# Optimization experiments

Measured on AMD Instinct MI355X. Metric: run time of the kernel, lower is better.

Reference implementation:

```python
import jax, jax.numpy as jnp
import numpy as np

B, I, S = 1024, 128, 512
UNFOLDS = 6


def setup_inputs() -> dict:
    key = jax.random.key(0)
    ks = jax.random.split(key, 16)
    inputs = jax.random.normal(ks[0], (B, I), dtype=jnp.float32)
    hx = jax.random.normal(ks[1], (B, S), dtype=jnp.float32)
    # learned parameters, initialized per _get_variables()
    input_w = jnp.ones((I,), dtype=jnp.float32)
    input_b = jnp.zeros((I,), dtype=jnp.float32)
    sensory_mu = jax.random.uniform(ks[2], (I, S)) * 0.5 + 0.3
    sensory_sigma = jax.random.uniform(ks[3], (I, S)) * 5.0 + 3.0
    sensory_W = jax.random.uniform(ks[4], (I, S), minval=0.01, maxval=1.0)
    sensory_erev = (2.0 * jax.random.randint(ks[5], (I, S), 0, 2) - 1.0).astype(jnp.float32)
    mu = jax.random.uniform(ks[6], (S, S)) * 0.5 + 0.3
    sigma = jax.random.uniform(ks[7], (S, S)) * 5.0 + 3.0
    W = jax.random.uniform(ks[8], (S, S), minval=0.01, maxval=1.0)
    erev = (2.0 * jax.random.randint(ks[9], (S, S), 0, 2) - 1.0).astype(jnp.float32)
    vleak = jax.random.uniform(ks[10], (S,)) * 0.4 - 0.2
    gleak = jnp.ones((S,), dtype=jnp.float32)   # gleak_init_min == gleak_init_max == 1
    cm_t = jnp.full((S,), 0.5, dtype=jnp.float32)  # cm_init_min == cm_init_max == 0.5
    return dict(inputs=inputs, hx=hx, input_w=input_w, input_b=input_b,
                sensory_mu=sensory_mu, sensory_sigma=sensory_sigma,
                sensory_W=sensory_W, sensory_erev=sensory_erev,
                mu=mu, sigma=sigma, W=W, erev=erev,
                vleak=vleak, gleak=gleak, cm_t=cm_t)


def reference(inputs, hx, input_w, input_b, sensory_mu, sensory_sigma,
              sensory_W, sensory_erev, mu, sigma, W, erev, vleak, gleak, cm_t):
    # Affine input mapping
    x = inputs * input_w + input_b                      # [B, I]
    # Sensory synapse activation (computed once): [B, I, S]
    sens_act = sensory_W * jax.nn.sigmoid(sensory_sigma * (x[:, :, None] - sensory_mu))
    w_num_sensory = jnp.sum(sens_act * sensory_erev, axis=1)  # [B, S]
    w_den_sensory = jnp.sum(sens_act, axis=1)                 # [B, S]

    v = hx
    for _ in range(UNFOLDS):
        # Recurrent synapse activation: broadcast state over presynaptic dim -> [B, S, S]
        w_act = W * jax.nn.sigmoid(sigma * (v[:, :, None] - mu))
        w_num = jnp.sum(w_act * erev, axis=1) + w_num_sensory   # [B, S]
        w_den = jnp.sum(w_act, axis=1) + w_den_sensory          # [B, S]
        numerator = cm_t * v + gleak * vleak + w_num
        denominator = cm_t + gleak + w_den
        v = numerator / denominator
    # forward returns (outputs, next_state), which are the same tensor
    return v
```

## Files before the change

### kernel.cpp

```cpp
#include <hip/hip_runtime.h>
#include <hip/hip_bf16.h>
#include <math.h>


#define B_TOT 1024
#define I_DIM 128
#define S_DIM 512
#define UNFOLDS 6
#define BT 4
#define TBL_N 4096
#define T_MAX 14.0f

__global__ __launch_bounds__(256) void prep_kernel(
    const float* __restrict__ sens_mu, const float* __restrict__ sens_sigma,
    const float* __restrict__ sens_W, const float* __restrict__ sens_erev,
    const float* __restrict__ mu, const float* __restrict__ sigma,
    const float* __restrict__ W, const float* __restrict__ erev,
    float4* __restrict__ recP, float4* __restrict__ sensP)
{
    const float L2E   = 1.4426950408889634f;
    const float SCALE = (float)TBL_N / (2.0f * T_MAX);
    const float OFF   = (float)(TBL_N / 2) + 0.5f;
    int idx = blockIdx.x * 256 + threadIdx.x;
    if (idx < I_DIM * S_DIM) {
        float sg = sens_sigma[idx], m = sens_mu[idx], w = sens_W[idx], er = sens_erev[idx];
        float A = -sg * L2E, C = sg * m * L2E;
        sensP[idx] = make_float4(A * SCALE, C * SCALE + OFF, w * er, w);
    }
    if (idx < S_DIM * S_DIM) {
        float sg = sigma[idx], m = mu[idx], w = W[idx], er = erev[idx];
        float A = -sg * L2E, C = sg * m * L2E;
        recP[idx] = make_float4(A * SCALE, C * SCALE + OFF, w * er, w);
    }
}

__global__ __launch_bounds__(512, 2) void liquid_main(
    const float* __restrict__ inputs,
    const float* __restrict__ hx,
    const float* __restrict__ input_w,
    const float* __restrict__ input_b,
    const float4* __restrict__ sensP,
    const float4* __restrict__ recP,
    const float* __restrict__ vleak,
    const float* __restrict__ gleak,
    const float* __restrict__ cm_t,
    float* __restrict__ out)
{
    const int j = threadIdx.x;
    const int b0 = blockIdx.x * BT;

    __shared__ float tbl[TBL_N];
    __shared__ float xs[BT][I_DIM];
    __shared__ float vs[BT][S_DIM];

    {
        const float INV_SCALE = (2.0f * T_MAX) / (float)TBL_N;
        for (int k = threadIdx.x; k < TBL_N; k += S_DIM) {
            float tc = ((float)k - (float)(TBL_N / 2)) * INV_SCALE;
            tbl[k] = 1.0f / (1.0f + exp2f(tc));
        }
    }

    {
        int b = threadIdx.x >> 7, ii = threadIdx.x & 127;
        xs[b][ii] = inputs[(b0 + b) * I_DIM + ii] * input_w[ii] + input_b[ii];
    }
    #pragma unroll
    for (int k = 0; k < BT; ++k)
        vs[k][j] = hx[(b0 + k) * S_DIM + j];
    __syncthreads();

    const float CLHI = (float)(TBL_N - 1);

    float snum[BT], sden[BT];
    #pragma unroll
    for (int b = 0; b < BT; ++b) { snum[b] = 0.f; sden[b] = 0.f; }

    for (int i = 0; i < I_DIM; i += 4) {
        float4 p[4];
        #pragma unroll
        for (int u = 0; u < 4; ++u) p[u] = sensP[(i + u) * S_DIM + j];
        #pragma unroll
        for (int b = 0; b < BT; ++b) {
            float4 xv4 = *(const float4*)&xs[b][i];
            float xv[4] = {xv4.x, xv4.y, xv4.z, xv4.w};
            #pragma unroll
            for (int u = 0; u < 4; ++u) {
                float f = fmaf(p[u].x, xv[u], p[u].y);
                f = __builtin_amdgcn_fmed3f(f, 0.0f, CLHI);
                float s = tbl[(unsigned)f];
                snum[b] = fmaf(p[u].z, s, snum[b]);
                sden[b] = fmaf(p[u].w, s, sden[b]);
            }
        }
    }

    const float gl = gleak[j], vl = vleak[j], cmj = cm_t[j];
    const float glvl = gl * vl;
    const float cg = cmj + gl;

    for (int it = 0; it < UNFOLDS; ++it) {
        float num[BT], den[BT];
        #pragma unroll
        for (int b = 0; b < BT; ++b) { num[b] = snum[b]; den[b] = sden[b]; }

        for (int i = 0; i < S_DIM; i += 4) {
            float4 p[4];
            #pragma unroll
            for (int u = 0; u < 4; ++u) p[u] = recP[(i + u) * S_DIM + j];
            #pragma unroll
            for (int b = 0; b < BT; ++b) {
                float4 vv4 = *(const float4*)&vs[b][i];
                float vv[4] = {vv4.x, vv4.y, vv4.z, vv4.w};
                #pragma unroll
                for (int u = 0; u < 4; ++u) {
                    float f = fmaf(p[u].x, vv[u], p[u].y);
                    f = __builtin_amdgcn_fmed3f(f, 0.0f, CLHI);
                    float s = tbl[(unsigned)f];
                    num[b] = fmaf(p[u].z, s, num[b]);
                    den[b] = fmaf(p[u].w, s, den[b]);
                }
            }
        }

        float vnew[BT];
        #pragma unroll
        for (int b = 0; b < BT; ++b) {
            float vold = vs[b][j];
            vnew[b] = (fmaf(cmj, vold, glvl) + num[b]) / (cg + den[b]);
        }
        __syncthreads();
        #pragma unroll
        for (int b = 0; b < BT; ++b) vs[b][j] = vnew[b];
        __syncthreads();
    }

    #pragma unroll
    for (int b = 0; b < BT; ++b)
        out[(b0 + b) * S_DIM + j] = vs[b][j];
}

extern "C" void kernel_launch(void* const* d_in, const int* in_sizes, int n_in,
                              void* d_out, int out_size, void* d_ws, size_t ws_size,
                              hipStream_t stream) {
    const float* inputs   = (const float*)d_in[0];
    const float* hx       = (const float*)d_in[1];
    const float* input_w  = (const float*)d_in[2];
    const float* input_b  = (const float*)d_in[3];
    const float* s_mu     = (const float*)d_in[4];
    const float* s_sigma  = (const float*)d_in[5];
    const float* s_W      = (const float*)d_in[6];
    const float* s_erev   = (const float*)d_in[7];
    const float* mu       = (const float*)d_in[8];
    const float* sigma    = (const float*)d_in[9];
    const float* W        = (const float*)d_in[10];
    const float* erev     = (const float*)d_in[11];
    const float* vleak    = (const float*)d_in[12];
    const float* gleak    = (const float*)d_in[13];
    const float* cm_t     = (const float*)d_in[14];
    float* out = (float*)d_out;

    float4* recP  = (float4*)d_ws;
    float4* sensP = (float4*)((char*)d_ws + (size_t)S_DIM * S_DIM * sizeof(float4));

    int prep_threads = S_DIM * S_DIM;
    prep_kernel<<<(prep_threads + 255) / 256, 256, 0, stream>>>(
        s_mu, s_sigma, s_W, s_erev, mu, sigma, W, erev, recP, sensP);

    liquid_main<<<B_TOT / BT, S_DIM, 0, stream>>>(
        inputs, hx, input_w, input_b, sensP, recP, vleak, gleak, cm_t, out);
}
```

Baseline: 423.7 us.

## Pack weights as fp16 pairs, replicate sigmoid table across LDS banks

Repacks the per-synapse parameters into 48-byte records that hold four float2 (A,C) pairs plus four fp16-packed (W*erev, W) pairs, and accumulates them with v_fma_mix_f32. This cuts global/L2 traffic per synapse from 16 to 12 bytes. The sigmoid lookup table is replicated 8 times and interleaved so each lane reads its own copy, which is meant to reduce LDS bank conflicts on the random-index gathers. The costs are a 128KB LDS table that limits occupancy to about one block per CU, with launch_bounds min-blocks dropped, and fp16 rounding of the weights.

```diff
diff --git a/kernel.cpp b/kernel.cpp
--- a/kernel.cpp
+++ b/kernel.cpp
@@ -1,5 +1,5 @@
 #include <hip/hip_runtime.h>
-#include <hip/hip_bf16.h>
+#include <hip/hip_fp16.h>
 #include <math.h>
 
 
@@ -9,89 +9,130 @@
 #define UNFOLDS 6
 #define BT 4
 #define TBL_N 4096
+#define NREP 8
 #define T_MAX 14.0f
+
+struct __align__(16) Rec {
+    float2   ac[4];
+    unsigned wh[4];
+};
 
 __global__ __launch_bounds__(256) void prep_kernel(
     const float* __restrict__ sens_mu, const float* __restrict__ sens_sigma,
     const float* __restrict__ sens_W, const float* __restrict__ sens_erev,
     const float* __restrict__ mu, const float* __restrict__ sigma,
     const float* __restrict__ W, const float* __restrict__ erev,
-    float4* __restrict__ recP, float4* __restrict__ sensP)
+    Rec* __restrict__ recG, Rec* __restrict__ sensG)
 {
     const float L2E   = 1.4426950408889634f;
     const float SCALE = (float)TBL_N / (2.0f * T_MAX);
     const float OFF   = (float)(TBL_N / 2) + 0.5f;
     int idx = blockIdx.x * 256 + threadIdx.x;
-    if (idx < I_DIM * S_DIM) {
-        float sg = sens_sigma[idx], m = sens_mu[idx], w = sens_W[idx], er = sens_erev[idx];
-        float A = -sg * L2E, C = sg * m * L2E;
-        sensP[idx] = make_float4(A * SCALE, C * SCALE + OFF, w * er, w);
-    }
-    if (idx < S_DIM * S_DIM) {
-        float sg = sigma[idx], m = mu[idx], w = W[idx], er = erev[idx];
-        float A = -sg * L2E, C = sg * m * L2E;
-        recP[idx] = make_float4(A * SCALE, C * SCALE + OFF, w * er, w);
-    }
-}
-
-__global__ __launch_bounds__(512, 2) void liquid_main(
+    int j = idx & (S_DIM - 1);
+    int g = idx >> 9;
+    if (g < S_DIM / 4) {
+        Rec r;
+        #pragma unroll
+        for (int u = 0; u < 4; ++u) {
+            int o = (g * 4 + u) * S_DIM + j;
+            float sg = sigma[o], m = mu[o], w = W[o], er = erev[o];
+            r.ac[u] = make_float2(-sg * L2E * SCALE, sg * m * L2E * SCALE + OFF);
+            __half2 h = __floats2half2_rn(w * er, w);
+            r.wh[u] = __builtin_bit_cast(unsigned, h);
+        }
+        recG[g * S_DIM + j] = r;
+    }
+    if (g < I_DIM / 4) {
+        Rec r;
+        #pragma unroll
+        for (int u = 0; u < 4; ++u) {
+            int o = (g * 4 + u) * S_DIM + j;
+            float sg = sens_sigma[o], m = sens_mu[o], w = sens_W[o], er = sens_erev[o];
+            r.ac[u] = make_float2(-sg * L2E * SCALE, sg * m * L2E * SCALE + OFF);
+            __half2 h = __floats2half2_rn(w * er, w);
+            r.wh[u] = __builtin_bit_cast(unsigned, h);
+        }
+        sensG[g * S_DIM + j] = r;
+    }
+}
+
+__device__ __forceinline__ void accum_group(
+    float4 q0, float4 q1, float4 q2, const float4* vv,
+    const char* tblL, float CLHI, float* num, float* den)
+{
+    float A[4]  = {q0.x, q0.z, q1.x, q1.z};
+    float C[4]  = {q0.y, q0.w, q1.y, q1.w};
+    unsigned wh[4] = {__float_as_uint(q2.x), __float_as_uint(q2.y),
+                      __float_as_uint(q2.z), __float_as_uint(q2.w)};
+    #pragma unroll
+    for (int u = 0; u < 4; ++u) {
+        #pragma unroll
+        for (int b = 0; b < BT; ++b) {
+            float vb = (u == 0) ? vv[b].x : (u == 1) ? vv[b].y
+                     : (u == 2) ? vv[b].z : vv[b].w;
+            float f = __builtin_amdgcn_fmed3f(fmaf(A[u], vb, C[u]), 0.0f, CLHI);
+            unsigned k = (unsigned)f;
+            float s = *(const float*)(tblL + (k << 5));
+            asm("v_fma_mix_f32 %0, %1, %2, %0 op_sel:[0,0,0] op_sel_hi:[1,0,0]"
+                : "+v"(num[b]) : "v"(wh[u]), "v"(s));
+            asm("v_fma_mix_f32 %0, %1, %2, %0 op_sel:[1,0,0] op_sel_hi:[1,0,0]"
+                : "+v"(den[b]) : "v"(wh[u]), "v"(s));
+        }
+    }
+}
+
+__global__ __launch_bounds__(512) void liquid_main(
     const float* __restrict__ inputs,
     const float* __restrict__ hx,
     const float* __restrict__ input_w,
     const float* __restrict__ input_b,
-    const float4* __restrict__ sensP,
-    const float4* __restrict__ recP,
+    const Rec* __restrict__ sensG,
+    const Rec* __restrict__ recG,
     const float* __restrict__ vleak,
     const float* __restrict__ gleak,
     const float* __restrict__ cm_t,
     float* __restrict__ out)
 {
+    __shared__ __align__(16) float tbl[TBL_N * NREP];
+    __shared__ __align__(16) float vsm[BT][S_DIM];
+    __shared__ __align__(16) float xsm[BT][I_DIM];
+
     const int j = threadIdx.x;
     const int b0 = blockIdx.x * BT;
 
-    __shared__ float tbl[TBL_N];
-    __shared__ float xs[BT][I_DIM];
-    __shared__ float vs[BT][S_DIM];
-
     {
-        const float INV_SCALE = (2.0f * T_MAX) / (float)TBL_N;
-        for (int k = threadIdx.x; k < TBL_N; k += S_DIM) {
-            float tc = ((float)k - (float)(TBL_N / 2)) * INV_SCALE;
-            tbl[k] = 1.0f / (1.0f + exp2f(tc));
-        }
-    }
-
+        const float INV = (2.0f * T_MAX) / (float)TBL_N;
+        for (int k = j; k < TBL_N; k += S_DIM) {
+            float s = 1.0f / (1.0f + exp2f((float)(k - TBL_N / 2) * INV));
+            #pragma unroll
+            for (int r = 0; r < NREP; ++r) tbl[k * NREP + r] = s;
+        }
+    }
     {
-        int b = threadIdx.x >> 7, ii = threadIdx.x & 127;
-        xs[b][ii] = inputs[(b0 + b) * I_DIM + ii] * input_w[ii] + input_b[ii];
-    }
-    #pragma unroll
-    for (int k = 0; k < BT; ++k)
-        vs[k][j] = hx[(b0 + k) * S_DIM + j];
+        int b = j >> 7, ii = j & 127;
+        xsm[b][ii] = inputs[(b0 + b) * I_DIM + ii] * input_w[ii] + input_b[ii];
+    }
+    #pragma unroll
+    for (int b = 0; b < BT; ++b)
+        vsm[b][j] = hx[(b0 + b) * S_DIM + j];
     __syncthreads();
 
+    const char* tblL = (const char*)(tbl + (j & (NREP - 1)));
     const float CLHI = (float)(TBL_N - 1);
 
     float snum[BT], sden[BT];
     #pragma unroll
     for (int b = 0; b < BT; ++b) { snum[b] = 0.f; sden[b] = 0.f; }
-
-    for (int i = 0; i < I_DIM; i += 4) {
-        float4 p[4];
-        #pragma unroll
-        for (int u = 0; u < 4; ++u) p[u] = sensP[(i + u) * S_DIM + j];
-        #pragma unroll
-        for (int b = 0; b < BT; ++b) {
-            float4 xv4 = *(const float4*)&xs[b][i];
-            float xv[4] = {xv4.x, xv4.y, xv4.z, xv4.w};
+    {
+        const float4* q = (const float4*)(sensG + j);
+        for (int g = 0; g < I_DIM / 4; ++g) {
+            float4 q0 = q[0], q1 = q[1], q2 = q[2];
+            q += 3 * S_DIM;
+            float4 xv[BT];
             #pragma unroll
-            for (int u = 0; u < 4; ++u) {
-                float f = fmaf(p[u].x, xv[u], p[u].y);
-                f = __builtin_amdgcn_fmed3f(f, 0.0f, CLHI);
-                float s = tbl[(unsigned)f];
-                snum[b] = fmaf(p[u].z, s, snum[b]);
-                sden[b] = fmaf(p[u].w, s, sden[b]);
-            }
+            for (int b = 0; b < BT; ++b)
+                xv[b] = *(const float4*)&xsm[b][g * 4];
+            accum_group(q0, q1, q2, xv, tblL, CLHI, snum, sden);
         }
     }
 
@@ -104,40 +145,32 @@
         #pragma unroll
         for (int b = 0; b < BT; ++b) { num[b] = snum[b]; den[b] = sden[b]; }
 
-        for (int i = 0; i < S_DIM; i += 4) {
-            float4 p[4];
+        const float4* q = (const float4*)(recG + j);
+        for (int g = 0; g < S_DIM / 4; ++g) {
+            float4 q0 = q[0], q1 = q[1], q2 = q[2];
+            q += 3 * S_DIM;
+            float4 vv[BT];
             #pragma unroll
-            for (int u = 0; u < 4; ++u) p[u] = recP[(i + u) * S_DIM + j];
-            #pragma unroll
-            for (int b = 0; b < BT; ++b) {
-                float4 vv4 = *(const float4*)&vs[b][i];
-                float vv[4] = {vv4.x, vv4.y, vv4.z, vv4.w};
-                #pragma unroll
-                for (int u = 0; u < 4; ++u) {
-                    float f = fmaf(p[u].x, vv[u], p[u].y);
-                    f = __builtin_amdgcn_fmed3f(f, 0.0f, CLHI);
-                    float s = tbl[(unsigned)f];
-                    num[b] = fmaf(p[u].z, s, num[b]);
-                    den[b] = fmaf(p[u].w, s, den[b]);
-                }
-            }
+            for (int b = 0; b < BT; ++b)
+                vv[b] = *(const float4*)&vsm[b][g * 4];
+            accum_group(q0, q1, q2, vv, tblL, CLHI, num, den);
         }
 
         float vnew[BT];
         #pragma unroll
         for (int b = 0; b < BT; ++b) {
-            float vold = vs[b][j];
+            float vold = vsm[b][j];
             vnew[b] = (fmaf(cmj, vold, glvl) + num[b]) / (cg + den[b]);
         }
         __syncthreads();
         #pragma unroll
-        for (int b = 0; b < BT; ++b) vs[b][j] = vnew[b];
+        for (int b = 0; b < BT; ++b) vsm[b][j] = vnew[b];
         __syncthreads();
     }
 
     #pragma unroll
     for (int b = 0; b < BT; ++b)
-        out[(b0 + b) * S_DIM + j] = vs[b][j];
+        out[(b0 + b) * S_DIM + j] = vsm[b][j];
 }
 
 extern "C" void kernel_launch(void* const* d_in, const int* in_sizes, int n_in,
@@ -160,13 +193,13 @@
     const float* cm_t     = (const float*)d_in[14];
     float* out = (float*)d_out;
 
-    float4* recP  = (float4*)d_ws;
-    float4* sensP = (float4*)((char*)d_ws + (size_t)S_DIM * S_DIM * sizeof(float4));
-
-    int prep_threads = S_DIM * S_DIM;
+    Rec* recG  = (Rec*)d_ws;
+    Rec* sensG = (Rec*)((char*)d_ws + (size_t)(S_DIM / 4) * S_DIM * sizeof(Rec));
+
+    int prep_threads = (S_DIM / 4) * S_DIM;
     prep_kernel<<<(prep_threads + 255) / 256, 256, 0, stream>>>(
-        s_mu, s_sigma, s_W, s_erev, mu, sigma, W, erev, recP, sensP);
+        s_mu, s_sigma, s_W, s_erev, mu, sigma, W, erev, recG, sensG);
 
     liquid_main<<<B_TOT / BT, S_DIM, 0, stream>>>(
-        inputs, hx, input_w, input_b, sensP, recP, vleak, gleak, cm_t, out);
-}
+        inputs, hx, input_w, input_b, sensG, recG, vleak, gleak, cm_t, out);
+}
```

Result: faster. 390.0 us (-8.0%).
